# Optimization experiments

Measured on AMD Instinct MI355X. Metric: run time of the kernel, lower is better.

The kernel has to match this reference:

```python
import jax, jax.numpy as jnp
import numpy as np

N_NODES = 100000
N_EDGES = 800000

def setup_inputs() -> dict:
    key = jax.random.key(0)
    ks = jax.random.split(key, 8)
    x = jax.random.normal(ks[0], (N_NODES, 500), dtype=jnp.float32)
    edge_index = jax.random.randint(ks[1], (2, N_EDGES), 0, N_NODES, dtype=jnp.int64)
    s = lambda k, shape, fan_in: jax.random.normal(k, shape, jnp.float32) / np.sqrt(fan_in)
    return {
        "x": x,
        "edge_index": edge_index,
        "W1_l": s(ks[2], (500, 20), 500),
        "W1_r": s(ks[3], (500, 20), 500),
        "b1": jnp.zeros((20,), jnp.float32),
        "W2_l": s(ks[4], (20, 3), 20),
        "W2_r": s(ks[5], (20, 3), 20),
        "b2": jnp.zeros((3,), jnp.float32),
    }

def _sage_conv(x, src, dst, W_l, W_r, b, deg_inv):
    # mean-aggregate neighbor features (x_j = x[src]) at dst, PyG default 'mean'
    agg = jax.ops.segment_sum(x[src], dst, num_segments=x.shape[0])  # [N, F]
    agg = agg * deg_inv[:, None]
    return agg @ W_l + b + x @ W_r

def reference(x, edge_index, W1_l, W1_r, b1, W2_l, W2_r, b2):
    src, dst = edge_index[0], edge_index[1]
    deg = jax.ops.segment_sum(jnp.ones_like(dst, dtype=x.dtype), dst, num_segments=x.shape[0])
    deg_inv = 1.0 / jnp.maximum(deg, 1.0)
    h = _sage_conv(x, src, dst, W1_l, W1_r, b1, deg_inv)
    h = jax.nn.relu(h)
    # F.dropout(p=0.5, training=self.training): identity in eval mode
    out = _sage_conv(h, src, dst, W2_l, W2_r, b2, deg_inv)
    return out
```

## Files before the change

kernel.cpp:

```cpp
#include <hip/hip_runtime.h>

#define F_IN  500
#define F_HID 20
#define F_OUT 3
#define KT    16
#define NT    3

typedef __attribute__((ext_vector_type(8))) short short8;
typedef __attribute__((ext_vector_type(4))) float v4f;

__device__ __forceinline__ unsigned f2bf(float f) {
    unsigned u = __float_as_uint(f);
    u = u + 0x7fffu + ((u >> 16) & 1u);
    return u >> 16;
}
__device__ __forceinline__ float bf2f(unsigned h) {
    return __uint_as_float(h << 16);
}

__device__ __forceinline__ void cvt8(const float4 p, const float4 q, short8& hi, short8& lo) {
    float vf[8] = {p.x, p.y, p.z, p.w, q.x, q.y, q.z, q.w};
    union { unsigned u[4]; short8 s; } H, L;
#pragma unroll
    for (int t = 0; t < 4; ++t) {
        unsigned u0 = __float_as_uint(vf[2*t]);
        unsigned u1 = __float_as_uint(vf[2*t+1]);
        unsigned r0 = u0 + 0x7fffu + ((u0 >> 16) & 1u);
        unsigned r1 = u1 + 0x7fffu + ((u1 >> 16) & 1u);
        float f0 = __uint_as_float(r0 & 0xffff0000u);
        float f1 = __uint_as_float(r1 & 0xffff0000u);
        float d0 = vf[2*t]   - f0;
        float d1 = vf[2*t+1] - f1;
        unsigned s0 = __float_as_uint(d0); s0 = s0 + 0x7fffu + ((s0 >> 16) & 1u);
        unsigned s1 = __float_as_uint(d1); s1 = s1 + 0x7fffu + ((s1 >> 16) & 1u);
        H.u[t] = (r0 >> 16) | (r1 & 0xffff0000u);
        L.u[t] = (s0 >> 16) | (s1 & 0xffff0000u);
    }
    hi = H.s; lo = L.s;
}

__global__ void k_prep(const float* __restrict__ W1l, const float* __restrict__ W1r,
                       unsigned short* __restrict__ Bhi, unsigned short* __restrict__ Blo,
                       const int* __restrict__ dst, int* __restrict__ deg, int E) {
    int b = blockIdx.x;
    int tid = threadIdx.x;
    if (b < (KT * NT * 64) / 256) {
        int i = b * 256 + tid;
        int lane = i & 63;
        int ntk  = i >> 6;
        int nt   = ntk % NT;
        int kt   = ntk / NT;
        int n     = nt * 16 + (lane & 15);
        int kbase = kt * 32 + (lane >> 4) * 8;
#pragma unroll
        for (int j = 0; j < 8; ++j) {
            int k = kbase + j;
            float w = 0.f;
            if (k < F_IN && n < 2 * F_HID)
                w = (n < F_HID) ? W1l[k * F_HID + n] : W1r[k * F_HID + (n - F_HID)];
            unsigned h = f2bf(w);
            Bhi[(size_t)i * 8 + j] = (unsigned short)h;
            Blo[(size_t)i * 8 + j] = (unsigned short)f2bf(w - bf2f(h));
        }
    } else {
        int e = (b - (KT * NT * 64) / 256) * 256 + tid;
        if (e < E) atomicAdd(&deg[dst[e]], 1);
    }
}

__global__ void k_scan_blk(const int* __restrict__ deg, int* __restrict__ rowloc,
                           int* __restrict__ blocksums, int N) {
    __shared__ int lds[256];
    int tid = threadIdx.x;
    int base = blockIdx.x * 1024 + tid * 4;
    int4 v = make_int4(0, 0, 0, 0);
    if (base + 3 < N) {
        v = *(const int4*)(deg + base);
    } else {
        if (base + 0 < N) v.x = deg[base + 0];
        if (base + 1 < N) v.y = deg[base + 1];
        if (base + 2 < N) v.z = deg[base + 2];
        if (base + 3 < N) v.w = deg[base + 3];
    }
    int tsum = v.x + v.y + v.z + v.w;
    lds[tid] = tsum;
    __syncthreads();
    for (int off = 1; off < 256; off <<= 1) {
        int t = (tid >= off) ? lds[tid - off] : 0;
        __syncthreads();
        lds[tid] += t;
        __syncthreads();
    }
    int excl = lds[tid] - tsum;
    if (tid == 255) blocksums[blockIdx.x] = lds[255];
    int r = excl;
    if (base + 0 < N) rowloc[base + 0] = r; r += v.x;
    if (base + 1 < N) rowloc[base + 1] = r; r += v.y;
    if (base + 2 < N) rowloc[base + 2] = r; r += v.z;
    if (base + 3 < N) rowloc[base + 3] = r;
}

__global__ void k_scan_sums(int* __restrict__ blocksums, int NB) {
    __shared__ int lds[256];
    int tid = threadIdx.x;
    int v = (tid < NB) ? blocksums[tid] : 0;
    lds[tid] = v;
    __syncthreads();
    for (int off = 1; off < 256; off <<= 1) {
        int t = (tid >= off) ? lds[tid - off] : 0;
        __syncthreads();
        lds[tid] += t;
        __syncthreads();
    }
    if (tid < NB) blocksums[tid] = lds[tid] - v;
}

__global__ void k_fill(const int* __restrict__ src, const int* __restrict__ dst,
                       int* __restrict__ rowloc, const int* __restrict__ bs,
                       int* __restrict__ csr, int E) {
    int e = blockIdx.x * blockDim.x + threadIdx.x;
    if (e >= E) return;
    int dn = dst[e];
    int pos = atomicAdd(&rowloc[dn], 1) + bs[dn >> 10];
    csr[pos] = src[e];
}

__global__ __launch_bounds__(256) void k_gemm1(const float* __restrict__ x,
        const unsigned short* __restrict__ Bhi, const unsigned short* __restrict__ Blo,
        float* __restrict__ yl, float* __restrict__ yr, int N) {
    const int lane = threadIdx.x & 63;
    const int wv   = threadIdx.x >> 6;
    const int fr   = lane & 15;
    const int kq   = lane >> 4;
    const int rowA = blockIdx.x * 128 + wv * 32;

    const int r0 = min(rowA + fr,      N - 1);
    const int r1 = min(rowA + 16 + fr, N - 1);
    const float* __restrict__ xp0 = x + (size_t)r0 * F_IN;
    const float* __restrict__ xp1 = x + (size_t)r1 * F_IN;

    v4f acc[2][NT];
#pragma unroll
    for (int h = 0; h < 2; ++h)
#pragma unroll
        for (int nt = 0; nt < NT; ++nt)
            acc[h][nt] = (v4f){0.f, 0.f, 0.f, 0.f};

#pragma unroll 2
    for (int kt = 0; kt < KT; ++kt) {
        const int kb = kt * 32 + kq * 8;
        const int ka = (kb     <= 496) ? kb     : 496;
        const int kc = (kb + 4 <= 496) ? kb + 4 : 496;
        float4 a0 = *(const float4*)(xp0 + ka);
        float4 a1 = *(const float4*)(xp0 + kc);
        float4 c0 = *(const float4*)(xp1 + ka);
        float4 c1 = *(const float4*)(xp1 + kc);
        short8 Ah0, Al0, Ah1, Al1;
        cvt8(a0, a1, Ah0, Al0);
        cvt8(c0, c1, Ah1, Al1);
#pragma unroll
        for (int nt = 0; nt < NT; ++nt) {
            size_t fo = (((size_t)kt * NT + nt) * 64 + lane) * 8;
            short8 Bh = *(const short8*)(Bhi + fo);
            short8 Bl = *(const short8*)(Blo + fo);
            acc[0][nt] = __builtin_amdgcn_mfma_f32_16x16x32_bf16(Ah0, Bh, acc[0][nt], 0, 0, 0);
            acc[0][nt] = __builtin_amdgcn_mfma_f32_16x16x32_bf16(Ah0, Bl, acc[0][nt], 0, 0, 0);
            acc[0][nt] = __builtin_amdgcn_mfma_f32_16x16x32_bf16(Al0, Bh, acc[0][nt], 0, 0, 0);
            acc[1][nt] = __builtin_amdgcn_mfma_f32_16x16x32_bf16(Ah1, Bh, acc[1][nt], 0, 0, 0);
            acc[1][nt] = __builtin_amdgcn_mfma_f32_16x16x32_bf16(Ah1, Bl, acc[1][nt], 0, 0, 0);
            acc[1][nt] = __builtin_amdgcn_mfma_f32_16x16x32_bf16(Al1, Bh, acc[1][nt], 0, 0, 0);
        }
    }
#pragma unroll
    for (int h = 0; h < 2; ++h) {
        int rbase = rowA + h * 16 + kq * 4;
#pragma unroll
        for (int nt = 0; nt < NT; ++nt) {
            int col = nt * 16 + fr;
            if (col < 2 * F_HID) {
#pragma unroll
                for (int rg = 0; rg < 4; ++rg) {
                    int grow = rbase + rg;
                    if (grow < N) {
                        if (col < F_HID) yl[(size_t)grow * 32 + col] = acc[h][nt][rg];
                        else             yr[(size_t)grow * F_HID + (col - F_HID)] = acc[h][nt][rg];
                    }
                }
            }
        }
    }
}

__global__ __launch_bounds__(256) void k_agg_l1(
        const int* __restrict__ rowloc, const int* __restrict__ bs,
        const int* __restrict__ deg, const int* __restrict__ csr,
        const float* __restrict__ yl, const float* __restrict__ yr,
        const float* __restrict__ b1, const float* __restrict__ W2l,
        const float* __restrict__ W2r,
        float* __restrict__ zl4, float* __restrict__ zr, int N) {
    int t = blockIdx.x * blockDim.x + threadIdx.x;
    int n = t >> 3;
    int g = t & 7;
    if (n >= N) return;
    int d   = deg[n];
    int end = rowloc[n] + bs[n >> 10];
    int beg = end - d;
    float4 a = make_float4(0.f, 0.f, 0.f, 0.f);
    if (g < 5) {
        for (int j = 0; j < d; ++j) {
            int s = csr[beg + j];
            float4 v = *(const float4*)(yl + (size_t)s * 32 + g * 4);
            a.x += v.x; a.y += v.y; a.z += v.z; a.w += v.w;
        }
    }
    float di = 1.0f / fmaxf((float)d, 1.0f);
    float pl0 = 0.f, pl1 = 0.f, pl2 = 0.f, pr0 = 0.f, pr1 = 0.f, pr2 = 0.f;
    if (g < 5) {
        float4 bb = *(const float4*)(b1 + g * 4);
        float4 rr = *(const float4*)(yr + (size_t)n * F_HID + g * 4);
        float h0 = fmaxf(a.x * di + bb.x + rr.x, 0.f);
        float h1 = fmaxf(a.y * di + bb.y + rr.y, 0.f);
        float h2 = fmaxf(a.z * di + bb.z + rr.z, 0.f);
        float h3 = fmaxf(a.w * di + bb.w + rr.w, 0.f);
        const float* wl = W2l + g * 4 * F_OUT;
        const float* wr = W2r + g * 4 * F_OUT;
        pl0 = h0 * wl[0] + h1 * wl[3] + h2 * wl[6] + h3 * wl[9];
        pl1 = h0 * wl[1] + h1 * wl[4] + h2 * wl[7] + h3 * wl[10];
        pl2 = h0 * wl[2] + h1 * wl[5] + h2 * wl[8] + h3 * wl[11];
        pr0 = h0 * wr[0] + h1 * wr[3] + h2 * wr[6] + h3 * wr[9];
        pr1 = h0 * wr[1] + h1 * wr[4] + h2 * wr[7] + h3 * wr[10];
        pr2 = h0 * wr[2] + h1 * wr[5] + h2 * wr[8] + h3 * wr[11];
    }
#pragma unroll
    for (int m = 4; m >= 1; m >>= 1) {
        pl0 += __shfl_xor(pl0, m);
        pl1 += __shfl_xor(pl1, m);
        pl2 += __shfl_xor(pl2, m);
        pr0 += __shfl_xor(pr0, m);
        pr1 += __shfl_xor(pr1, m);
        pr2 += __shfl_xor(pr2, m);
    }
    if (g == 0) {
        *(float4*)(zl4 + (size_t)n * 4) = make_float4(pl0, pl1, pl2, 0.f);
        zr[(size_t)n * 3 + 0] = pr0;
        zr[(size_t)n * 3 + 1] = pr1;
        zr[(size_t)n * 3 + 2] = pr2;
    }
}

__global__ void k_agg2_final(const int* __restrict__ rowloc, const int* __restrict__ bs,
                             const int* __restrict__ deg, const int* __restrict__ csr,
                             const float* __restrict__ zl4, const float* __restrict__ zr,
                             const float* __restrict__ b2, float* __restrict__ out, int N) {
    int n = blockIdx.x * blockDim.x + threadIdx.x;
    if (n >= N) return;
    int d   = deg[n];
    int end = rowloc[n] + bs[n >> 10];
    int beg = end - d;
    float a0 = 0.f, a1 = 0.f, a2 = 0.f;
    for (int j = 0; j < d; ++j) {
        int s = csr[beg + j];
        float4 z = *(const float4*)(zl4 + (size_t)s * 4);
        a0 += z.x; a1 += z.y; a2 += z.z;
    }
    float di = 1.0f / fmaxf((float)d, 1.0f);
    out[(size_t)n * F_OUT + 0] = a0 * di + b2[0] + zr[(size_t)n * 3 + 0];
    out[(size_t)n * F_OUT + 1] = a1 * di + b2[1] + zr[(size_t)n * 3 + 1];
    out[(size_t)n * F_OUT + 2] = a2 * di + b2[2] + zr[(size_t)n * 3 + 2];
}

extern "C" void kernel_launch(void* const* d_in, const int* in_sizes, int n_in,
                              void* d_out, int out_size, void* d_ws, size_t ws_size,
                              hipStream_t stream) {
    const float* x   = (const float*)d_in[0];
    const int*   ei  = (const int*)d_in[1];
    const float* W1l = (const float*)d_in[2];
    const float* W1r = (const float*)d_in[3];
    const float* b1  = (const float*)d_in[4];
    const float* W2l = (const float*)d_in[5];
    const float* W2r = (const float*)d_in[6];
    const float* b2  = (const float*)d_in[7];
    float* out = (float*)d_out;

    const int N = in_sizes[0] / F_IN;
    const int E = in_sizes[1] / 2;
    const int* src = ei;
    const int* dst = ei + E;

    int*   wsi    = (int*)d_ws;
    int*   deg    = wsi;
    int*   rowloc = deg + N;
    int*   bs     = rowloc + N;
    int*   csr    = bs + 256;
    float* yl     = (float*)(csr + E);
    float* yr     = yl + (size_t)N * 32;
    float* zl4    = yr + (size_t)N * F_HID;
    float* zr     = zl4 + (size_t)N * 4;
    unsigned short* Bhi = (unsigned short*)(zr + (size_t)N * F_OUT);
    unsigned short* Blo = Bhi + (size_t)KT * NT * 64 * 8;

    hipMemsetAsync(deg, 0, (size_t)N * sizeof(int), stream);

    const int B = 256;
    const int NB = (N + 1023) / 1024;
    k_prep      <<<(KT * NT * 64) / B + (E + B - 1) / B, B, 0, stream>>>(W1l, W1r, Bhi, Blo, dst, deg, E);
    k_scan_blk  <<<NB, 256, 0, stream>>>(deg, rowloc, bs, N);
    k_scan_sums <<<1, 256, 0, stream>>>(bs, NB);
    k_fill      <<<(E + B - 1) / B, B, 0, stream>>>(src, dst, rowloc, bs, csr, E);
    k_gemm1     <<<(N + 127) / 128, 256, 0, stream>>>(x, Bhi, Blo, yl, yr, N);
    k_agg_l1    <<<(N * 8 + B - 1) / B, B, 0, stream>>>(rowloc, bs, deg, csr, yl, yr, b1, W2l, W2r, zl4, zr, N);
    k_agg2_final<<<(N + B - 1) / B, B, 0, stream>>>(rowloc, bs, deg, csr, zl4, zr, b2, out, N);
}
```

Measured before the change: 447.6 us.

## Fuse scan passes with grid barrier and merge CSR fill into GEMM launch

Merges the two-pass prefix scan into one kernel that uses an atomic counter spin-barrier across its 98 blocks, so every block can add the preceding block sums and write absolute row starts. The CSR fill is moved into extra blocks of the GEMM launch so the fill scatter overlaps with the dense GEMM, and the row offsets no longer need a separate block-sum lookup. This removes two kernel launches and lets the atomic-heavy fill hide behind GEMM memory traffic. The spin barrier assumes all scan blocks are resident at once, and the fill blocks compete with the GEMM blocks for bandwidth.

Measured after the change: 422.5 us. 1.06x faster.

```diff
diff --git a/kernel.cpp b/kernel.cpp
--- a/kernel.cpp
+++ b/kernel.cpp
@@ -68,11 +68,13 @@
     }
 }
 
-__global__ void k_scan_blk(const int* __restrict__ deg, int* __restrict__ rowloc,
-                           int* __restrict__ blocksums, int N) {
+__global__ __launch_bounds__(256) void k_scan(const int* __restrict__ deg,
+        int* __restrict__ rowstart, int* __restrict__ bs, int* __restrict__ ctr,
+        int N, int NB) {
     __shared__ int lds[256];
     int tid = threadIdx.x;
-    int base = blockIdx.x * 1024 + tid * 4;
+    int b   = blockIdx.x;
+    int base = b * 1024 + tid * 4;
     int4 v = make_int4(0, 0, 0, 0);
     if (base + 3 < N) {
         v = *(const int4*)(deg + base);
@@ -91,43 +93,46 @@
         lds[tid] += t;
         __syncthreads();
     }
-    int excl = lds[tid] - tsum;
-    if (tid == 255) blocksums[blockIdx.x] = lds[255];
-    int r = excl;
-    if (base + 0 < N) rowloc[base + 0] = r; r += v.x;
-    if (base + 1 < N) rowloc[base + 1] = r; r += v.y;
-    if (base + 2 < N) rowloc[base + 2] = r; r += v.z;
-    if (base + 3 < N) rowloc[base + 3] = r;
-}
-
-__global__ void k_scan_sums(int* __restrict__ blocksums, int NB) {
-    __shared__ int lds[256];
-    int tid = threadIdx.x;
-    int v = (tid < NB) ? blocksums[tid] : 0;
-    lds[tid] = v;
+    int excl  = lds[tid] - tsum;
+    int total = lds[255];
     __syncthreads();
-    for (int off = 1; off < 256; off <<= 1) {
-        int t = (tid >= off) ? lds[tid - off] : 0;
+    if (tid == 0) {
+        atomicExch(&bs[b], total);
+        __threadfence();
+        atomicAdd(ctr, 1);
+        while (atomicAdd(ctr, 0) < NB) __builtin_amdgcn_s_sleep(2);
+        __threadfence();
+    }
+    __syncthreads();
+    int sb = (tid < b) ? atomicAdd(&bs[tid], 0) : 0;
+    lds[tid] = sb;
+    __syncthreads();
+    for (int off = 128; off > 0; off >>= 1) {
+        if (tid < off) lds[tid] += lds[tid + off];
         __syncthreads();
-        lds[tid] += t;
-        __syncthreads();
-    }
-    if (tid < NB) blocksums[tid] = lds[tid] - v;
-}
-
-__global__ void k_fill(const int* __restrict__ src, const int* __restrict__ dst,
-                       int* __restrict__ rowloc, const int* __restrict__ bs,
-                       int* __restrict__ csr, int E) {
-    int e = blockIdx.x * blockDim.x + threadIdx.x;
-    if (e >= E) return;
-    int dn = dst[e];
-    int pos = atomicAdd(&rowloc[dn], 1) + bs[dn >> 10];
-    csr[pos] = src[e];
-}
-
-__global__ __launch_bounds__(256) void k_gemm1(const float* __restrict__ x,
+    }
+    int r = lds[0] + excl;
+    if (base + 0 < N) rowstart[base + 0] = r; r += v.x;
+    if (base + 1 < N) rowstart[base + 1] = r; r += v.y;
+    if (base + 2 < N) rowstart[base + 2] = r; r += v.z;
+    if (base + 3 < N) rowstart[base + 3] = r;
+}
+
+__global__ __launch_bounds__(256) void k_gemm_fill(const float* __restrict__ x,
         const unsigned short* __restrict__ Bhi, const unsigned short* __restrict__ Blo,
-        float* __restrict__ yl, float* __restrict__ yr, int N) {
+        float* __restrict__ yl, float* __restrict__ yr,
+        const int* __restrict__ src, const int* __restrict__ dst,
+        int* __restrict__ rowstart, int* __restrict__ csr,
+        int N, int E, int GB) {
+    if ((int)blockIdx.x >= GB) {
+        int e = ((int)blockIdx.x - GB) * 256 + (int)threadIdx.x;
+        if (e < E) {
+            int dn = dst[e];
+            int pos = atomicAdd(&rowstart[dn], 1);
+            csr[pos] = src[e];
+        }
+        return;
+    }
     const int lane = threadIdx.x & 63;
     const int wv   = threadIdx.x >> 6;
     const int fr   = lane & 15;
@@ -192,8 +197,8 @@
 }
 
 __global__ __launch_bounds__(256) void k_agg_l1(
-        const int* __restrict__ rowloc, const int* __restrict__ bs,
-        const int* __restrict__ deg, const int* __restrict__ csr,
+        const int* __restrict__ rowend, const int* __restrict__ deg,
+        const int* __restrict__ csr,
         const float* __restrict__ yl, const float* __restrict__ yr,
         const float* __restrict__ b1, const float* __restrict__ W2l,
         const float* __restrict__ W2r,
@@ -203,8 +208,7 @@
     int g = t & 7;
     if (n >= N) return;
     int d   = deg[n];
-    int end = rowloc[n] + bs[n >> 10];
-    int beg = end - d;
+    int beg = rowend[n] - d;
     float4 a = make_float4(0.f, 0.f, 0.f, 0.f);
     if (g < 5) {
         for (int j = 0; j < d; ++j) {
@@ -248,15 +252,14 @@
     }
 }
 
-__global__ void k_agg2_final(const int* __restrict__ rowloc, const int* __restrict__ bs,
-                             const int* __restrict__ deg, const int* __restrict__ csr,
+__global__ void k_agg2_final(const int* __restrict__ rowend, const int* __restrict__ deg,
+                             const int* __restrict__ csr,
                              const float* __restrict__ zl4, const float* __restrict__ zr,
                              const float* __restrict__ b2, float* __restrict__ out, int N) {
     int n = blockIdx.x * blockDim.x + threadIdx.x;
     if (n >= N) return;
     int d   = deg[n];
-    int end = rowloc[n] + bs[n >> 10];
-    int beg = end - d;
+    int beg = rowend[n] - d;
     float a0 = 0.f, a1 = 0.f, a2 = 0.f;
     for (int j = 0; j < d; ++j) {
         int s = csr[beg + j];
@@ -287,27 +290,31 @@
     const int* src = ei;
     const int* dst = ei + E;
 
-    int*   wsi    = (int*)d_ws;
-    int*   deg    = wsi;
-    int*   rowloc = deg + N;
-    int*   bs     = rowloc + N;
-    int*   csr    = bs + 256;
-    float* yl     = (float*)(csr + E);
-    float* yr     = yl + (size_t)N * 32;
-    float* zl4    = yr + (size_t)N * F_HID;
-    float* zr     = zl4 + (size_t)N * 4;
+    int*   wsi      = (int*)d_ws;
+    int*   deg      = wsi;
+    int*   ctr      = deg + N;
+    int*   rowstart = ctr + 16;
+    int*   bs       = rowstart + N;
+    int*   csr      = bs + 256;
+    float* yl       = (float*)(csr + E);
+    float* yr       = yl + (size_t)N * 32;
+    float* zl4      = yr + (size_t)N * F_HID;
+    float* zr       = zl4 + (size_t)N * 4;
     unsigned short* Bhi = (unsigned short*)(zr + (size_t)N * F_OUT);
     unsigned short* Blo = Bhi + (size_t)KT * NT * 64 * 8;
 
-    hipMemsetAsync(deg, 0, (size_t)N * sizeof(int), stream);
-
-    const int B = 256;
+    hipMemsetAsync(deg, 0, ((size_t)N + 16) * sizeof(int), stream);
+
+    const int B  = 256;
     const int NB = (N + 1023) / 1024;
-    k_prep      <<<(KT * NT * 64) / B + (E + B - 1) / B, B, 0, stream>>>(W1l, W1r, Bhi, Blo, dst, deg, E);
-    k_scan_blk  <<<NB, 256, 0, stream>>>(deg, rowloc, bs, N);
-    k_scan_sums <<<1, 256, 0, stream>>>(bs, NB);
-    k_fill      <<<(E + B - 1) / B, B, 0, stream>>>(src, dst, rowloc, bs, csr, E);
-    k_gemm1     <<<(N + 127) / 128, 256, 0, stream>>>(x, Bhi, Blo, yl, yr, N);
-    k_agg_l1    <<<(N * 8 + B - 1) / B, B, 0, stream>>>(rowloc, bs, deg, csr, yl, yr, b1, W2l, W2r, zl4, zr, N);
-    k_agg2_final<<<(N + B - 1) / B, B, 0, stream>>>(rowloc, bs, deg, csr, zl4, zr, b2, out, N);
-}
+    const int PB = (KT * NT * 64) / B;
+    const int DB = (E + B - 1) / B;
+    const int GB = (N + 127) / 128;
+    const int FB = (E + B - 1) / B;
+
+    k_prep      <<<PB + DB, B, 0, stream>>>(W1l, W1r, Bhi, Blo, dst, deg, E);
+    k_scan      <<<NB, 256, 0, stream>>>(deg, rowstart, bs, ctr, N, NB);
+    k_gemm_fill <<<GB + FB, B, 0, stream>>>(x, Bhi, Blo, yl, yr, src, dst, rowstart, csr, N, E, GB);
+    k_agg_l1    <<<(N * 8 + B - 1) / B, B, 0, stream>>>(rowstart, deg, csr, yl, yr, b1, W2l, W2r, zl4, zr, N);
+    k_agg2_final<<<(N + B - 1) / B, B, 0, stream>>>(rowstart, deg, csr, zl4, zr, b2, out, N);
+}
```
